# Performance work log

Measured on AMD Instinct MI355X. Metric: run time of the kernel, lower is better.

Reference implementation:

```python
import jax, jax.numpy as jnp
import numpy as np

N = 8192       # batch size
BIT = 32       # hash code length
NCLASS = 100   # number of classes
ALPHA = 0.1    # config['alpha'] (quantization weight)
BEITA = 1.0    # config['beita'] (classification weight)
GAMMA = 0.1    # config['gamma'] (balancing weight)
P = 2          # config['p']


def setup_inputs() -> dict:
    key = jax.random.key(0)
    k1, k2, k3 = jax.random.split(key, 3)
    u = jax.random.normal(k1, (N, BIT), dtype=jnp.float32)
    Y = jax.random.normal(k2, (N, NCLASS), dtype=jnp.float32)
    labels = jax.random.randint(k3, (N,), 0, NCLASS)
    y = jax.nn.one_hot(labels, NCLASS, dtype=jnp.float32)  # one-hot targets
    return {"u": u, "Y": Y, "y": y}


def _hash_loss(u, y):
    n = u.shape[0]
    theta = (u @ u.T) * 0.5                       # [N, N]
    sim = (y @ y.T > 0).astype(u.dtype)           # [N, N] pairwise same-class
    # log(1 + exp(theta)) - Sim * theta  (logaddexp = stable same math)
    pair = jnp.logaddexp(0.0, theta) - sim * theta
    mask_pos = sim > 0
    s1 = sim.sum() - n                            # positives minus diagonal
    s0 = n * n - sim.sum()                        # negatives
    s0 = jnp.where(s0 == 0, 1.0, s0)
    s1 = jnp.where(s1 == 0, 1.0, s1)
    s = s0 + s1
    scale = jnp.where(mask_pos, s / s1, s / s0)
    pair = pair * scale
    # original subtracts diag of the *detached* rescaled matrix
    pair = pair - jax.lax.stop_gradient(jnp.diag(jnp.diag(pair)))
    count = n * (n - 1) / 2
    return pair.sum() / 2.0 / count


def reference(u, Y, y):
    likelihood_loss = _hash_loss(u, y)
    # CrossEntropyLoss with soft (one-hot float) targets
    logp = jax.nn.log_softmax(Y, axis=-1)
    classification_loss = -(y * logp).sum(axis=-1).mean()
    m = u.mean(axis=1)
    if P == 1:
        quantization_loss = ALPHA * jnp.abs(m).mean()
    else:
        quantization_loss = ALPHA * (m ** 2).mean()
    b = jnp.sign(u)
    balancing_loss = GAMMA * ((u - b) ** 2).mean()
    return likelihood_loss + BEITA * classification_loss + quantization_loss + balancing_loss
```

## Files before the change

### kernel.cpp

```cpp
#include <hip/hip_runtime.h>
#include <math.h>
#include <type_traits>

#define N 8192
#define BIT 32
#define NCLASS 100
#define ALPHA 0.1
#define BEITA 1.0
#define GAMMA 0.1

#define BT 256
#define NT (N / BT)
#define NPAIRBLK (NT * (NT + 1) / 2)
#define NPREP (N / 8)

typedef __attribute__((ext_vector_type(8))) short s16x8;
typedef __attribute__((ext_vector_type(4))) float f32x4;

static __device__ __forceinline__ unsigned short f2bf(float f) {
    unsigned int x = __float_as_uint(f);
    x += 0x7fff + ((x >> 16) & 1);
    return (unsigned short)(x >> 16);
}


__global__ __launch_bounds__(256) void prep_kernel(
    const float* __restrict__ u, const float* __restrict__ Y, const float* __restrict__ y,
    int* __restrict__ labels, double* __restrict__ Pc, double* __restrict__ Pm,
    double* __restrict__ Pb)
{
    const int t = threadIdx.x;
    const int lane = t & 63;
    const int w = t >> 6;
    const int row0 = blockIdx.x * 8;

    float wcls = 0.f;
    #pragma unroll
    for (int rr = 0; rr < 2; ++rr) {
        const int r = row0 + w * 2 + rr;
        const float* Yp = Y + (size_t)r * NCLASS;
        const float* yp = y + (size_t)r * NCLASS;
        const bool has2 = lane < (NCLASS - 64);
        float Y0 = Yp[lane];
        float Y1 = has2 ? Yp[64 + lane] : -1e30f;
        float y0 = yp[lane];
        float y1 = has2 ? yp[64 + lane] : 0.f;
        float m = fmaxf(Y0, Y1);
        #pragma unroll
        for (int o = 32; o; o >>= 1) m = fmaxf(m, __shfl_xor(m, o, 64));
        float e  = __expf(Y0 - m) + (has2 ? __expf(Y1 - m) : 0.f);
        float tg = y0 * Y0 + (has2 ? y1 * Y1 : 0.f);
        #pragma unroll
        for (int o = 32; o; o >>= 1) { e += __shfl_xor(e, o, 64); tg += __shfl_xor(tg, o, 64); }
        unsigned long long b0 = __ballot(y0 > 0.5f);
        unsigned long long b1 = __ballot(has2 && (y1 > 0.5f));
        if (lane == 0) {
            int lbl = b0 ? (__ffsll((long long)b0) - 1) : (64 + __ffsll((long long)b1) - 1);
            labels[r] = lbl;
            wcls += m + __logf(e) - tg;
        }
    }

    const float x = u[(size_t)row0 * BIT + t];
    float bb = (x > 0.f) ? 1.f : ((x < 0.f) ? -1.f : 0.f);
    float d = x - bb;
    float bal = d * d;
    float rs = x;
    #pragma unroll
    for (int o = 1; o < 32; o <<= 1) rs += __shfl_xor(rs, o, 64);
    float mrow = rs * (1.f / BIT);
    float m2 = ((t & 31) == 0) ? mrow * mrow : 0.f;
    #pragma unroll
    for (int o = 32; o; o >>= 1) { m2 += __shfl_down(m2, o, 64); bal += __shfl_down(bal, o, 64); }

    __shared__ double red[4][3];
    if (lane == 0) { red[w][0] = (double)wcls; red[w][1] = (double)m2; red[w][2] = (double)bal; }
    __syncthreads();
    if (t == 0) {
        Pc[blockIdx.x] = red[0][0] + red[1][0] + red[2][0] + red[3][0];
        Pm[blockIdx.x] = red[0][1] + red[1][1] + red[2][1] + red[3][1];
        Pb[blockIdx.x] = red[0][2] + red[1][2] + red[2][2] + red[3][2];
    }
}

__global__ __launch_bounds__(256) void pair_kernel(
    const float* __restrict__ u, const int* __restrict__ labels,
    double* __restrict__ Ppos, double* __restrict__ Pneg)
{
    const int b = blockIdx.x;
    int ti = (int)(((float)(2 * NT + 1) - sqrtf((float)((2 * NT + 1) * (2 * NT + 1) - 8 * b))) * 0.5f);
    int S = ti * (2 * NT - ti + 1) / 2;
    if (S > b) { --ti; S = ti * (2 * NT - ti + 1) / 2; }
    else { int S2 = (ti + 1) * (2 * NT - ti) / 2; if (S2 <= b) { ++ti; S = S2; } }
    const int tj = ti + (b - S);
    const int i0 = ti * BT, j0 = tj * BT;

    __shared__ __align__(16) unsigned short Us[4][512][8];
    __shared__ int Ls[512];
    __shared__ float wredp[4], wredn[4];

    const int t = threadIdx.x;

    #pragma unroll
    for (int h = 0; h < 2; ++h) {
        const int sr = t + h * 256;
        const int g  = (h == 0) ? (i0 + t) : (j0 + t);
        const float4* p = (const float4*)(u + (size_t)g * BIT);
        #pragma unroll
        for (int c = 0; c < 4; ++c) {
            float4 v0 = p[2 * c], v1 = p[2 * c + 1];
            s16x8 fr;
            fr[0] = (short)f2bf(v0.x); fr[1] = (short)f2bf(v0.y);
            fr[2] = (short)f2bf(v0.z); fr[3] = (short)f2bf(v0.w);
            fr[4] = (short)f2bf(v1.x); fr[5] = (short)f2bf(v1.y);
            fr[6] = (short)f2bf(v1.z); fr[7] = (short)f2bf(v1.w);
            *(s16x8*)&Us[c][sr][0] = fr;
        }
        Ls[sr] = labels[g];
    }
    __syncthreads();

    const int lane = t & 63;
    const int w = t >> 6;
    const int wy = w >> 1, wx = w & 1;
    const int quad = lane >> 4, lr = lane & 15;

    float sp0 = 0.f, sp1 = 0.f, sn0 = 0.f, sn1 = 0.f;
    auto run = [&](auto DIAGC) {
        constexpr bool DIAG = decltype(DIAGC)::value;
        #pragma unroll 1
        for (int ga = 0; ga < 2; ++ga) {
            s16x8 av[4];
            #pragma unroll
            for (int a = 0; a < 4; ++a)
                av[a] = *(const s16x8*)&Us[quad][wy * 128 + ga * 64 + a * 16 + lr][0];
            int lav[16];
            #pragma unroll
            for (int a = 0; a < 4; ++a)
                #pragma unroll
                for (int r = 0; r < 4; ++r)
                    lav[a * 4 + r] = Ls[wy * 128 + ga * 64 + a * 16 + quad * 4 + r];

            #pragma unroll 1
            for (int gb = 0; gb < 2; ++gb) {
                s16x8 bv[4];
                #pragma unroll
                for (int c = 0; c < 4; ++c)
                    bv[c] = *(const s16x8*)&Us[quad][256 + wx * 128 + gb * 64 + c * 16 + lr][0];
                int lbv[4];
                #pragma unroll
                for (int c = 0; c < 4; ++c)
                    lbv[c] = Ls[256 + wx * 128 + gb * 64 + c * 16 + lr];

                f32x4 accf[4][4];
                #pragma unroll
                for (int a = 0; a < 4; ++a)
                    #pragma unroll
                    for (int c = 0; c < 4; ++c)
                        accf[a][c] = __builtin_amdgcn_mfma_f32_16x16x32_bf16(
                            av[a], bv[c], (f32x4){0.f, 0.f, 0.f, 0.f}, 0, 0, 0);

                #pragma unroll
                for (int a = 0; a < 4; ++a) {
                    #pragma unroll
                    for (int c = 0; c < 4; ++c) {
                        const int lb = lbv[c];
                        #pragma unroll
                        for (int r = 0; r < 4; ++r) {
                            const float v = accf[a][c][r];
                            const bool sim = (lav[a * 4 + r] == lb);
                            float hv = 0.5f * v;
                            float e  = exp2f(-1.44269504f * fabsf(hv));
                            float lt = 0.69314718f * __log2f(1.f + e);
                            float tp = fmaxf(-hv, 0.f) + lt;
                            float tn = fmaxf(hv, 0.f) + lt;
                            if (DIAG) {
                                const int lrow = wy * 128 + ga * 64 + a * 16 + quad * 4 + r;
                                const int lcol = wx * 128 + gb * 64 + c * 16 + lr;
                                const bool keep = lcol > lrow;
                                tp = keep ? tp : 0.f;
                                tn = keep ? tn : 0.f;
                            }
                            float up = sim ? tp : 0.f;
                            float un = sim ? 0.f : tn;
                            if (r & 1) { sp1 += up; sn1 += un; }
                            else       { sp0 += up; sn0 += un; }
                        }
                    }
                }
            }
        }
    };
    if (ti == tj) run(std::integral_constant<bool, true>{});
    else          run(std::integral_constant<bool, false>{});

    float sp = sp0 + sp1, sn = sn0 + sn1;
    #pragma unroll
    for (int o = 32; o; o >>= 1) { sp += __shfl_down(sp, o, 64); sn += __shfl_down(sn, o, 64); }
    if (lane == 0) { wredp[w] = sp; wredn[w] = sn; }
    __syncthreads();
    if (t == 0) {
        Ppos[b] = (double)(wredp[0] + wredp[1] + wredp[2] + wredp[3]);
        Pneg[b] = (double)(wredn[0] + wredn[1] + wredn[2] + wredn[3]);
    }
}

__global__ __launch_bounds__(256) void fin_kernel(
    const int* __restrict__ labels, const double* __restrict__ Ppos,
    const double* __restrict__ Pneg, const double* __restrict__ Pc,
    const double* __restrict__ Pm, const double* __restrict__ Pb, float* __restrict__ out)
{
    __shared__ int h[128];
    __shared__ double red[4][5];
    __shared__ double scd[2];
    const int t = threadIdx.x;
    const int lane = t & 63;
    const int w = t >> 6;

    if (t < 128) h[t] = 0;
    __syncthreads();
    #pragma unroll
    for (int k = 0; k < 32; ++k) atomicAdd(&h[labels[t + k * 256]], 1);
    __syncthreads();

    if (w == 0) {
        long long c0 = (lane < NCLASS) ? h[lane] : 0;
        long long c1 = (lane + 64 < NCLASS) ? h[lane + 64] : 0;
        long long ss = c0 * c0 + c1 * c1;
        #pragma unroll
        for (int o = 32; o; o >>= 1) ss += __shfl_xor(ss, o, 64);
        if (lane == 0) {
            double s1 = (double)ss - (double)N;
            double s0 = (double)N * (double)N - (double)ss;
            if (s0 == 0.0) s0 = 1.0;
            if (s1 == 0.0) s1 = 1.0;
            double s = s0 + s1;
            scd[0] = s / s1;
            scd[1] = s / s0;
        }
    }

    double p0 = 0, p1 = 0, cc = 0, mm = 0, bb = 0;
    for (int i = t; i < NPAIRBLK; i += 256) { p0 += Ppos[i]; p1 += Pneg[i]; }
    for (int i = t; i < NPREP; i += 256)    { cc += Pc[i]; mm += Pm[i]; bb += Pb[i]; }
    #pragma unroll
    for (int o = 32; o; o >>= 1) {
        p0 += __shfl_down(p0, o, 64); p1 += __shfl_down(p1, o, 64);
        cc += __shfl_down(cc, o, 64); mm += __shfl_down(mm, o, 64);
        bb += __shfl_down(bb, o, 64);
    }
    if (lane == 0) { red[w][0] = p0; red[w][1] = p1; red[w][2] = cc; red[w][3] = mm; red[w][4] = bb; }
    __syncthreads();
    if (t == 0) {
        double a_pos = red[0][0] + red[1][0] + red[2][0] + red[3][0];
        double a_neg = red[0][1] + red[1][1] + red[2][1] + red[3][1];
        double a_cls = red[0][2] + red[1][2] + red[2][2] + red[3][2];
        double a_m2  = red[0][3] + red[1][3] + red[2][3] + red[3][3];
        double a_bal = red[0][4] + red[1][4] + red[2][4] + red[3][4];
        double pairsum = scd[0] * a_pos + scd[1] * a_neg;
        double lik   = 2.0 * pairsum / ((double)N * (double)(N - 1));
        double cls   = a_cls / (double)N;
        double quant = ALPHA * (a_m2 / (double)N);
        double bal   = GAMMA * (a_bal / ((double)N * (double)BIT));
        out[0] = (float)(lik + BEITA * cls + quant + bal);
    }
}

extern "C" void kernel_launch(void* const* d_in, const int* in_sizes, int n_in,
                              void* d_out, int out_size, void* d_ws, size_t ws_size,
                              hipStream_t stream) {
    const float* u = (const float*)d_in[0];
    const float* Y = (const float*)d_in[1];
    const float* y = (const float*)d_in[2];
    float* out = (float*)d_out;

    char* ws = (char*)d_ws;
    int*    labels = (int*)(ws + 1024);
    double* Ppos   = (double*)(ws + 40960);
    double* Pneg   = (double*)(ws + 49152);
    double* Pc     = (double*)(ws + 57344);
    double* Pm     = (double*)(ws + 65536);
    double* Pb     = (double*)(ws + 73728);

    prep_kernel<<<NPREP, 256, 0, stream>>>(u, Y, y, labels, Pc, Pm, Pb);
    pair_kernel<<<NPAIRBLK, 256, 0, stream>>>(u, labels, Ppos, Pneg);
    fin_kernel<<<1, 256, 0, stream>>>(labels, Ppos, Pneg, Pc, Pm, Pb, out);
}
```

Measured before the change: 110.1 us.

## Use 512-thread blocks in pair kernel with 2x4 wave grid and hoisted B fragments

The pair kernel now launches 512 threads per block and arranges its 8 waves as a 2x4 grid. Each wave covers 64 columns instead of 128, so its B fragments and labels load once outside the loop and the inner gb loop disappears. The staging loop collapses to one row per thread, and the negative term is computed as tp + hv instead of a second max. This spreads the transcendental-heavy work over more waves to hide latency, at the cost of higher register pressure under the (512,4) launch bounds.

Result: faster. 104.9 us (-4.7%).

```diff
diff --git a/kernel.cpp b/kernel.cpp
--- a/kernel.cpp
+++ b/kernel.cpp
@@ -83,7 +83,7 @@
     }
 }
 
-__global__ __launch_bounds__(256) void pair_kernel(
+__global__ __launch_bounds__(512, 4) void pair_kernel(
     const float* __restrict__ u, const int* __restrict__ labels,
     double* __restrict__ Ppos, double* __restrict__ Pneg)
 {
@@ -97,14 +97,12 @@
 
     __shared__ __align__(16) unsigned short Us[4][512][8];
     __shared__ int Ls[512];
-    __shared__ float wredp[4], wredn[4];
+    __shared__ float wredp[8], wredn[8];
 
     const int t = threadIdx.x;
 
-    #pragma unroll
-    for (int h = 0; h < 2; ++h) {
-        const int sr = t + h * 256;
-        const int g  = (h == 0) ? (i0 + t) : (j0 + t);
+    {
+        const int g = (t < 256) ? (i0 + t) : (j0 + t - 256);
         const float4* p = (const float4*)(u + (size_t)g * BIT);
         #pragma unroll
         for (int c = 0; c < 4; ++c) {
@@ -114,16 +112,24 @@
             fr[2] = (short)f2bf(v0.z); fr[3] = (short)f2bf(v0.w);
             fr[4] = (short)f2bf(v1.x); fr[5] = (short)f2bf(v1.y);
             fr[6] = (short)f2bf(v1.z); fr[7] = (short)f2bf(v1.w);
-            *(s16x8*)&Us[c][sr][0] = fr;
-        }
-        Ls[sr] = labels[g];
+            *(s16x8*)&Us[c][t][0] = fr;
+        }
+        Ls[t] = labels[g];
     }
     __syncthreads();
 
     const int lane = t & 63;
     const int w = t >> 6;
-    const int wy = w >> 1, wx = w & 1;
+    const int wy = w >> 2, wx = w & 3;
     const int quad = lane >> 4, lr = lane & 15;
+
+    s16x8 bv[4];
+    int lbv[4];
+    #pragma unroll
+    for (int c = 0; c < 4; ++c) {
+        bv[c]  = *(const s16x8*)&Us[quad][256 + wx * 64 + c * 16 + lr][0];
+        lbv[c] = Ls[256 + wx * 64 + c * 16 + lr];
+    }
 
     float sp0 = 0.f, sp1 = 0.f, sn0 = 0.f, sn1 = 0.f;
     auto run = [&](auto DIAGC) {
@@ -141,51 +147,39 @@
                 for (int r = 0; r < 4; ++r)
                     lav[a * 4 + r] = Ls[wy * 128 + ga * 64 + a * 16 + quad * 4 + r];
 
-            #pragma unroll 1
-            for (int gb = 0; gb < 2; ++gb) {
-                s16x8 bv[4];
+            f32x4 accf[4][4];
+            #pragma unroll
+            for (int a = 0; a < 4; ++a)
                 #pragma unroll
                 for (int c = 0; c < 4; ++c)
-                    bv[c] = *(const s16x8*)&Us[quad][256 + wx * 128 + gb * 64 + c * 16 + lr][0];
-                int lbv[4];
+                    accf[a][c] = __builtin_amdgcn_mfma_f32_16x16x32_bf16(
+                        av[a], bv[c], (f32x4){0.f, 0.f, 0.f, 0.f}, 0, 0, 0);
+
+            #pragma unroll
+            for (int a = 0; a < 4; ++a) {
                 #pragma unroll
-                for (int c = 0; c < 4; ++c)
-                    lbv[c] = Ls[256 + wx * 128 + gb * 64 + c * 16 + lr];
-
-                f32x4 accf[4][4];
-                #pragma unroll
-                for (int a = 0; a < 4; ++a)
+                for (int c = 0; c < 4; ++c) {
+                    const int lb = lbv[c];
                     #pragma unroll
-                    for (int c = 0; c < 4; ++c)
-                        accf[a][c] = __builtin_amdgcn_mfma_f32_16x16x32_bf16(
-                            av[a], bv[c], (f32x4){0.f, 0.f, 0.f, 0.f}, 0, 0, 0);
-
-                #pragma unroll
-                for (int a = 0; a < 4; ++a) {
-                    #pragma unroll
-                    for (int c = 0; c < 4; ++c) {
-                        const int lb = lbv[c];
-                        #pragma unroll
-                        for (int r = 0; r < 4; ++r) {
-                            const float v = accf[a][c][r];
-                            const bool sim = (lav[a * 4 + r] == lb);
-                            float hv = 0.5f * v;
-                            float e  = exp2f(-1.44269504f * fabsf(hv));
-                            float lt = 0.69314718f * __log2f(1.f + e);
-                            float tp = fmaxf(-hv, 0.f) + lt;
-                            float tn = fmaxf(hv, 0.f) + lt;
-                            if (DIAG) {
-                                const int lrow = wy * 128 + ga * 64 + a * 16 + quad * 4 + r;
-                                const int lcol = wx * 128 + gb * 64 + c * 16 + lr;
-                                const bool keep = lcol > lrow;
-                                tp = keep ? tp : 0.f;
-                                tn = keep ? tn : 0.f;
-                            }
-                            float up = sim ? tp : 0.f;
-                            float un = sim ? 0.f : tn;
-                            if (r & 1) { sp1 += up; sn1 += un; }
-                            else       { sp0 += up; sn0 += un; }
+                    for (int r = 0; r < 4; ++r) {
+                        const float v = accf[a][c][r];
+                        const bool sim = (lav[a * 4 + r] == lb);
+                        float hv = 0.5f * v;
+                        float e  = exp2f(-1.44269504f * fabsf(hv));
+                        float lt = 0.69314718f * __log2f(1.f + e);
+                        float tp = fmaxf(-hv, 0.f) + lt;
+                        float tn = tp + hv;
+                        if (DIAG) {
+                            const int lrow = wy * 128 + ga * 64 + a * 16 + quad * 4 + r;
+                            const int lcol = wx * 64 + c * 16 + lr;
+                            const bool keep = lcol > lrow;
+                            tp = keep ? tp : 0.f;
+                            tn = keep ? tn : 0.f;
                         }
+                        float up = sim ? tp : 0.f;
+                        float un = sim ? 0.f : tn;
+                        if (r & 1) { sp1 += up; sn1 += un; }
+                        else       { sp0 += up; sn0 += un; }
                     }
                 }
             }
@@ -200,8 +194,11 @@
     if (lane == 0) { wredp[w] = sp; wredn[w] = sn; }
     __syncthreads();
     if (t == 0) {
-        Ppos[b] = (double)(wredp[0] + wredp[1] + wredp[2] + wredp[3]);
-        Pneg[b] = (double)(wredn[0] + wredn[1] + wredn[2] + wredn[3]);
+        float fp = 0.f, fn = 0.f;
+        #pragma unroll
+        for (int i = 0; i < 8; ++i) { fp += wredp[i]; fn += wredn[i]; }
+        Ppos[b] = (double)fp;
+        Pneg[b] = (double)fn;
     }
 }
 
@@ -283,6 +280,6 @@
     double* Pb     = (double*)(ws + 73728);
 
     prep_kernel<<<NPREP, 256, 0, stream>>>(u, Y, y, labels, Pc, Pm, Pb);
-    pair_kernel<<<NPAIRBLK, 256, 0, stream>>>(u, labels, Ppos, Pneg);
+    pair_kernel<<<NPAIRBLK, 512, 0, stream>>>(u, labels, Ppos, Pneg);
     fin_kernel<<<1, 256, 0, stream>>>(labels, Ppos, Pneg, Pc, Pm, Pb, out);
 }
```
